# Performance work log

Measured on AMD Instinct MI355X. Metric: run time of the kernel, lower is better.

The kernel has to match this reference:

```python
import jax, jax.numpy as jnp
import numpy as np
import math

B, S, E, H = 2, 4096, 1024, 1024

def setup_inputs() -> dict:
    key = jax.random.key(0)
    ks = jax.random.split(key, 7)
    X = jax.random.normal(ks[0], (B, S, E), dtype=jnp.float32)
    attention_mask = jnp.ones((B, S, S), dtype=jnp.int32)
    sc = 1.0 / math.sqrt(E)
    Wq = jax.random.normal(ks[1], (H, E), dtype=jnp.float32) * sc
    Wk = jax.random.normal(ks[2], (H, E), dtype=jnp.float32) * sc
    Wv = jax.random.normal(ks[3], (H, E), dtype=jnp.float32) * sc
    bq = jnp.zeros((H,), dtype=jnp.float32)
    bk = jnp.zeros((H,), dtype=jnp.float32)
    bv = jnp.zeros((H,), dtype=jnp.float32)
    return {"X": X, "attention_mask": attention_mask,
            "Wq": Wq, "bq": bq, "Wk": Wk, "bk": bk, "Wv": Wv, "bv": bv}

def reference(X, attention_mask, Wq, bq, Wk, bk, Wv, bv):
    # Linear layers: y = x @ W^T + b (torch convention W is [out, in])
    Q = jnp.einsum('bse,he->bsh', X, Wq) + bq
    K = jnp.einsum('bse,he->bsh', X, Wk) + bk
    V = jnp.einsum('bse,he->bsh', X, Wv) + bv
    scale = 1.0 / math.sqrt(H)
    scores = jnp.einsum('bqh,bkh->bqk', Q, K) * scale  # [B,S,S]
    scores = jnp.where(attention_mask == 0, -jnp.inf, scores)
    # dropout (eval mode -> identity) would be applied here, BEFORE softmax
    weights = jax.nn.softmax(scores, axis=-1)
    out = jnp.einsum('bqk,bkh->bqh', weights, V)  # [B,S,H]
    return out
```

## Files before the change

kernel.cpp:

```cpp
#include <hip/hip_runtime.h>
#include <stdint.h>


typedef __bf16 bf16;
typedef __attribute__((ext_vector_type(4))) __bf16 bf16x4;
typedef __attribute__((ext_vector_type(8))) __bf16 bf16x8;
typedef __attribute__((ext_vector_type(4))) float f32x4;
typedef __attribute__((ext_vector_type(4))) int i32x4;

__device__ __forceinline__ void g2l16(const void* g, void* l) {
  __builtin_amdgcn_global_load_lds(
      (const __attribute__((address_space(1))) uint32_t*)g,
      (__attribute__((address_space(3))) uint32_t*)l, 16, 0, 0);
}

__global__ __launch_bounds__(256) void cvt_f32_bf16(
    const float* __restrict__ src, bf16* __restrict__ dst, int n) {
  const int i = (blockIdx.x * 256 + threadIdx.x) * 8;
  if (i >= n) return;
  f32x4 a = *(const f32x4*)(src + i);
  f32x4 b = *(const f32x4*)(src + i + 4);
  bf16x8 o;
#pragma unroll
  for (int e = 0; e < 4; ++e) { o[e] = (bf16)a[e]; o[4 + e] = (bf16)b[e]; }
  *(bf16x8*)(dst + i) = o;
}

__global__ __launch_bounds__(256) void cvt_w3(
    const float* __restrict__ Wq, const float* __restrict__ Wk,
    const float* __restrict__ Wv, bf16* __restrict__ dst) {
  const int i = (blockIdx.x * 256 + threadIdx.x) * 8;
  const int seg = i >> 20;
  const int off = i & 1048575;
  const float* src = (seg == 0) ? Wq : (seg == 1) ? Wk : Wv;
  f32x4 a = *(const f32x4*)(src + off);
  f32x4 b = *(const f32x4*)(src + off + 4);
  bf16x8 o;
#pragma unroll
  for (int e = 0; e < 4; ++e) { o[e] = (bf16)a[e]; o[4 + e] = (bf16)b[e]; }
  *(bf16x8*)(dst + i) = o;
}


__global__ __launch_bounds__(256, 2) void gemm_qkv(
    const bf16* __restrict__ Xb, const bf16* __restrict__ Wb3,
    const float* __restrict__ bq, const float* __restrict__ bk,
    const float* __restrict__ bv, bf16* __restrict__ QK,
    bf16* __restrict__ Vt)
{
  constexpr int K = 1024, N = 1024;
  __shared__ __align__(16) bf16 ldsA[128 * 64];
  __shared__ __align__(16) bf16 ldsB[128 * 64];

  const int tid  = threadIdx.x;
  const int lane = tid & 63;
  const int wave = tid >> 6;
  const int which = blockIdx.y >> 3;
  const int n0 = (blockIdx.y & 7) * 128;
  const int m0 = blockIdx.x * 128;
  const bf16* Bt = Wb3 + (size_t)which * 1048576;
  const float* bias = (which == 0) ? bq : ((which == 1) ? bk : bv);

  const int l15  = lane & 15;
  const int quad = lane >> 4;
  const int wm = (wave >> 1) * 64;
  const int wn = (wave & 1) * 64;
  const int sw = l15 & 7;

  f32x4 acc[4][4];
#pragma unroll
  for (int i = 0; i < 4; ++i)
#pragma unroll
    for (int j = 0; j < 4; ++j) acc[i][j] = f32x4{0.f, 0.f, 0.f, 0.f};

  const int srow = tid >> 3;
  const int scol = ((tid & 7) ^ (srow & 7)) * 8;
  const size_t a_base = (size_t)(m0 + srow) * K + scol;
  const size_t b_base = (size_t)(n0 + srow) * K + scol;
  const int lds_off = tid * 8;

  for (int kt = 0; kt < K; kt += 64) {
    const bf16* ga = Xb + a_base + kt;
    const bf16* gb = Bt + b_base + kt;
#pragma unroll
    for (int it = 0; it < 4; ++it) {
      g2l16(ga + (size_t)(it * 32) * K, &ldsA[lds_off + it * 2048]);
      g2l16(gb + (size_t)(it * 32) * K, &ldsB[lds_off + it * 2048]);
    }
    __syncthreads();
#pragma unroll
    for (int ks = 0; ks < 2; ++ks) {
      const int ch = ks * 4 + quad;
      bf16x8 af[4], bfg[4];
#pragma unroll
      for (int i = 0; i < 4; ++i)
        af[i] = *(const bf16x8*)&ldsA[(wm + i * 16 + l15) * 64 + (ch ^ sw) * 8];
#pragma unroll
      for (int j = 0; j < 4; ++j)
        bfg[j] = *(const bf16x8*)&ldsB[(wn + j * 16 + l15) * 64 + (ch ^ sw) * 8];
#pragma unroll
      for (int i = 0; i < 4; ++i)
#pragma unroll
        for (int j = 0; j < 4; ++j)
          acc[i][j] = __builtin_amdgcn_mfma_f32_16x16x32_bf16(
              af[i], bfg[j], acc[i][j], 0, 0, 0);
    }
    __syncthreads();
  }

  if (which < 2) {
    bf16* C = QK + (size_t)which * (size_t)(8192 * 1024);
#pragma unroll
    for (int i = 0; i < 4; ++i) {
#pragma unroll
      for (int j = 0; j < 4; ++j) {
        const int r = m0 + wm + i * 16 + quad * 4;
        const int c = n0 + wn + j * 16 + l15;
        const float bvv = bias[c];
        f32x4 v = acc[i][j];
#pragma unroll
        for (int reg = 0; reg < 4; ++reg)
          C[(size_t)(r + reg) * N + c] = (bf16)(v[reg] + bvv);
      }
    }
  } else {
#pragma unroll
    for (int i = 0; i < 4; ++i) {
#pragma unroll
      for (int j = 0; j < 4; ++j) {
        const int r = m0 + wm + i * 16 + quad * 4;
        const int c = n0 + wn + j * 16 + l15;
        const int b = r >> 12, s = r & 4095;
        const float bvv = bias[c];
        f32x4 v = acc[i][j];
        bf16x4 o;
#pragma unroll
        for (int reg = 0; reg < 4; ++reg) o[reg] = (bf16)(v[reg] + bvv);
        *(bf16x4*)&Vt[((size_t)(b * 1024 + c)) * 4096 + s] = o;
      }
    }
  }
}

template <typename CT>
__global__ __launch_bounds__(256, 2) void gemm_bt(
    const bf16* __restrict__ A, const bf16* __restrict__ Bt,
    CT* __restrict__ C, int M, int N, int K, long long bt_batch_stride,
    float scale)
{
  __shared__ __align__(16) bf16 ldsA[128 * 64];
  __shared__ __align__(16) bf16 ldsB[128 * 64];

  const int tid  = threadIdx.x;
  const int lane = tid & 63;
  const int wave = tid >> 6;
  const int m0 = blockIdx.x * 128;
  const int n0 = blockIdx.y * 128;
  const int batch = m0 >> 12;
  const bf16* Btb = Bt + (size_t)batch * (size_t)bt_batch_stride;

  const int l15  = lane & 15;
  const int quad = lane >> 4;
  const int wm = (wave >> 1) * 64;
  const int wn = (wave & 1) * 64;
  const int sw = l15 & 7;

  f32x4 acc[4][4];
#pragma unroll
  for (int i = 0; i < 4; ++i)
#pragma unroll
    for (int j = 0; j < 4; ++j) acc[i][j] = f32x4{0.f, 0.f, 0.f, 0.f};

  const int srow = tid >> 3;
  const int scol = ((tid & 7) ^ (srow & 7)) * 8;
  const size_t a_base = (size_t)(m0 + srow) * K + scol;
  const size_t b_base = (size_t)(n0 + srow) * K + scol;
  const int lds_off = tid * 8;

  for (int kt = 0; kt < K; kt += 64) {
    const bf16* ga = A + a_base + kt;
    const bf16* gb = Btb + b_base + kt;
#pragma unroll
    for (int it = 0; it < 4; ++it) {
      g2l16(ga + (size_t)(it * 32) * K, &ldsA[lds_off + it * 2048]);
      g2l16(gb + (size_t)(it * 32) * K, &ldsB[lds_off + it * 2048]);
    }
    __syncthreads();
#pragma unroll
    for (int ks = 0; ks < 2; ++ks) {
      const int ch = ks * 4 + quad;
      bf16x8 af[4], bfg[4];
#pragma unroll
      for (int i = 0; i < 4; ++i)
        af[i] = *(const bf16x8*)&ldsA[(wm + i * 16 + l15) * 64 + (ch ^ sw) * 8];
#pragma unroll
      for (int j = 0; j < 4; ++j)
        bfg[j] = *(const bf16x8*)&ldsB[(wn + j * 16 + l15) * 64 + (ch ^ sw) * 8];
#pragma unroll
      for (int i = 0; i < 4; ++i)
#pragma unroll
        for (int j = 0; j < 4; ++j)
          acc[i][j] = __builtin_amdgcn_mfma_f32_16x16x32_bf16(
              af[i], bfg[j], acc[i][j], 0, 0, 0);
    }
    __syncthreads();
  }

#pragma unroll
  for (int i = 0; i < 4; ++i) {
#pragma unroll
    for (int j = 0; j < 4; ++j) {
      const int r = m0 + wm + i * 16 + quad * 4;
      const int c = n0 + wn + j * 16 + l15;
      f32x4 v = acc[i][j];
#pragma unroll
      for (int reg = 0; reg < 4; ++reg)
        C[(size_t)(r + reg) * N + c] = (CT)(v[reg] * scale);
    }
  }
}

__global__ __launch_bounds__(256) void softmax_rows(
    bf16* __restrict__ Sc, const int* __restrict__ mask) {
  const int row = blockIdx.x;
  bf16* p = Sc + (size_t)row * 4096;
  const int* mrow = mask + (size_t)row * 4096;
  const int tid = threadIdx.x;
  const int wave = tid >> 6;

  const bf16x8* pv = (const bf16x8*)p;
  bf16x8 v0 = pv[tid * 2];
  bf16x8 v1 = pv[tid * 2 + 1];
  const i32x4* mv = (const i32x4*)mrow;
  i32x4 mk[4];
#pragma unroll
  for (int q = 0; q < 4; ++q) mk[q] = mv[tid * 4 + q];

  float x[16];
#pragma unroll
  for (int i = 0; i < 8; ++i) {
    x[i] = (float)v0[i];
    x[8 + i] = (float)v1[i];
  }
#pragma unroll
  for (int i = 0; i < 16; ++i)
    if (mk[i >> 2][i & 3] == 0) x[i] = -30000.0f;

  float m = -30000.0f;
#pragma unroll
  for (int i = 0; i < 16; ++i) m = fmaxf(m, x[i]);
#pragma unroll
  for (int off = 1; off < 64; off <<= 1) m = fmaxf(m, __shfl_xor(m, off));
  __shared__ float red[4];
  if ((tid & 63) == 0) red[wave] = m;
  __syncthreads();
  m = fmaxf(fmaxf(red[0], red[1]), fmaxf(red[2], red[3]));

  float s = 0.f;
#pragma unroll
  for (int i = 0; i < 16; ++i) {
    x[i] = __expf(x[i] - m);
    s += x[i];
  }
#pragma unroll
  for (int off = 1; off < 64; off <<= 1) s += __shfl_xor(s, off);
  __syncthreads();
  if ((tid & 63) == 0) red[wave] = s;
  __syncthreads();
  s = red[0] + red[1] + red[2] + red[3];
  const float inv = 1.0f / s;

  bf16x8 o0, o1;
#pragma unroll
  for (int i = 0; i < 8; ++i) {
    o0[i] = (bf16)(x[i] * inv);
    o1[i] = (bf16)(x[8 + i] * inv);
  }
  bf16x8* pw = (bf16x8*)p;
  pw[tid * 2] = o0;
  pw[tid * 2 + 1] = o1;
}

extern "C" void kernel_launch(void* const* d_in, const int* in_sizes, int n_in,
                              void* d_out, int out_size, void* d_ws,
                              size_t ws_size, hipStream_t stream) {
  const float* X   = (const float*)d_in[0];
  const int* mask  = (const int*)d_in[1];
  const float* Wq  = (const float*)d_in[2];
  const float* bq  = (const float*)d_in[3];
  const float* Wk  = (const float*)d_in[4];
  const float* bk  = (const float*)d_in[5];
  const float* Wv  = (const float*)d_in[6];
  const float* bv  = (const float*)d_in[7];
  float* out = (float*)d_out;

  const size_t QKV_ELEMS = (size_t)8192 * 1024;
  bf16* Q    = (bf16*)d_ws;
  bf16* Kb   = Q + QKV_ELEMS;
  bf16* X_bf = Kb + QKV_ELEMS;
  bf16* Vt   = X_bf + QKV_ELEMS;
  bf16* Sc   = Vt + QKV_ELEMS;
  bf16* W_bf = Sc;

  const dim3 blk(256);
  cvt_f32_bf16<<<dim3(4096), blk, 0, stream>>>(X, X_bf, 8388608);
  cvt_w3<<<dim3(1536), blk, 0, stream>>>(Wq, Wk, Wv, W_bf);
  gemm_qkv<<<dim3(64, 24), blk, 0, stream>>>(X_bf, W_bf, bq, bk, bv, Q, Vt);
  gemm_bt<bf16><<<dim3(64, 32), blk, 0, stream>>>(
      Q, Kb, Sc, 8192, 4096, 1024, 4096LL * 1024LL, 0.03125f);
  softmax_rows<<<dim3(8192), blk, 0, stream>>>(Sc, mask);
  gemm_bt<float><<<dim3(64, 8), blk, 0, stream>>>(
      Sc, Vt, out, 8192, 1024, 4096, 1024LL * 4096LL, 1.0f);
}
```

Measured before the change: 432.6 us.

## Fuse mask and exp into score GEMM epilogue, defer normalization to PV GEMM

```diff
diff --git a/kernel.cpp b/kernel.cpp
--- a/kernel.cpp
+++ b/kernel.cpp
@@ -6,7 +6,6 @@
 typedef __attribute__((ext_vector_type(4))) __bf16 bf16x4;
 typedef __attribute__((ext_vector_type(8))) __bf16 bf16x8;
 typedef __attribute__((ext_vector_type(4))) float f32x4;
-typedef __attribute__((ext_vector_type(4))) int i32x4;
 
 __device__ __forceinline__ void g2l16(const void* g, void* l) {
   __builtin_amdgcn_global_load_lds(
@@ -142,12 +141,12 @@
   }
 }
 
-template <typename CT>
-__global__ __launch_bounds__(256, 2) void gemm_bt(
+__global__ __launch_bounds__(256, 2) void gemm_scores(
     const bf16* __restrict__ A, const bf16* __restrict__ Bt,
-    CT* __restrict__ C, int M, int N, int K, long long bt_batch_stride,
-    float scale)
+    const int* __restrict__ mask, bf16* __restrict__ P,
+    float* __restrict__ row_sum)
 {
+  constexpr int N = 4096, K = 1024;
   __shared__ __align__(16) bf16 ldsA[128 * 64];
   __shared__ __align__(16) bf16 ldsB[128 * 64];
 
@@ -157,7 +156,7 @@
   const int m0 = blockIdx.x * 128;
   const int n0 = blockIdx.y * 128;
   const int batch = m0 >> 12;
-  const bf16* Btb = Bt + (size_t)batch * (size_t)bt_batch_stride;
+  const bf16* Btb = Bt + (size_t)batch * (size_t)(4096 * 1024);
 
   const int l15  = lane & 15;
   const int quad = lane >> 4;
@@ -208,77 +207,112 @@
 
 #pragma unroll
   for (int i = 0; i < 4; ++i) {
+    const int r = m0 + wm + i * 16 + quad * 4;
+    f32x4 rsum = f32x4{0.f, 0.f, 0.f, 0.f};
 #pragma unroll
     for (int j = 0; j < 4; ++j) {
-      const int r = m0 + wm + i * 16 + quad * 4;
       const int c = n0 + wn + j * 16 + l15;
       f32x4 v = acc[i][j];
 #pragma unroll
+      for (int reg = 0; reg < 4; ++reg) {
+        float e = __expf(v[reg] * 0.03125f);
+        if (mask[(size_t)(r + reg) * N + c] == 0) e = 0.f;
+        P[(size_t)(r + reg) * N + c] = (bf16)e;
+        rsum[reg] += e;
+      }
+    }
+#pragma unroll
+    for (int off = 1; off < 16; off <<= 1) {
+#pragma unroll
       for (int reg = 0; reg < 4; ++reg)
-        C[(size_t)(r + reg) * N + c] = (CT)(v[reg] * scale);
-    }
-  }
-}
-
-__global__ __launch_bounds__(256) void softmax_rows(
-    bf16* __restrict__ Sc, const int* __restrict__ mask) {
-  const int row = blockIdx.x;
-  bf16* p = Sc + (size_t)row * 4096;
-  const int* mrow = mask + (size_t)row * 4096;
-  const int tid = threadIdx.x;
+        rsum[reg] += __shfl_xor(rsum[reg], off);
+    }
+    if (l15 == 0) {
+#pragma unroll
+      for (int reg = 0; reg < 4; ++reg)
+        atomicAdd(&row_sum[r + reg], rsum[reg]);
+    }
+  }
+}
+
+__global__ __launch_bounds__(256, 2) void gemm_pv(
+    const bf16* __restrict__ A, const bf16* __restrict__ Bt,
+    const float* __restrict__ row_sum, float* __restrict__ C)
+{
+  constexpr int N = 1024, K = 4096;
+  __shared__ __align__(16) bf16 ldsA[128 * 64];
+  __shared__ __align__(16) bf16 ldsB[128 * 64];
+
+  const int tid  = threadIdx.x;
+  const int lane = tid & 63;
   const int wave = tid >> 6;
-
-  const bf16x8* pv = (const bf16x8*)p;
-  bf16x8 v0 = pv[tid * 2];
-  bf16x8 v1 = pv[tid * 2 + 1];
-  const i32x4* mv = (const i32x4*)mrow;
-  i32x4 mk[4];
-#pragma unroll
-  for (int q = 0; q < 4; ++q) mk[q] = mv[tid * 4 + q];
-
-  float x[16];
-#pragma unroll
-  for (int i = 0; i < 8; ++i) {
-    x[i] = (float)v0[i];
-    x[8 + i] = (float)v1[i];
-  }
-#pragma unroll
-  for (int i = 0; i < 16; ++i)
-    if (mk[i >> 2][i & 3] == 0) x[i] = -30000.0f;
-
-  float m = -30000.0f;
-#pragma unroll
-  for (int i = 0; i < 16; ++i) m = fmaxf(m, x[i]);
-#pragma unroll
-  for (int off = 1; off < 64; off <<= 1) m = fmaxf(m, __shfl_xor(m, off));
-  __shared__ float red[4];
-  if ((tid & 63) == 0) red[wave] = m;
-  __syncthreads();
-  m = fmaxf(fmaxf(red[0], red[1]), fmaxf(red[2], red[3]));
-
-  float s = 0.f;
-#pragma unroll
-  for (int i = 0; i < 16; ++i) {
-    x[i] = __expf(x[i] - m);
-    s += x[i];
-  }
-#pragma unroll
-  for (int off = 1; off < 64; off <<= 1) s += __shfl_xor(s, off);
-  __syncthreads();
-  if ((tid & 63) == 0) red[wave] = s;
-  __syncthreads();
-  s = red[0] + red[1] + red[2] + red[3];
-  const float inv = 1.0f / s;
-
-  bf16x8 o0, o1;
-#pragma unroll
-  for (int i = 0; i < 8; ++i) {
-    o0[i] = (bf16)(x[i] * inv);
-    o1[i] = (bf16)(x[8 + i] * inv);
-  }
-  bf16x8* pw = (bf16x8*)p;
-  pw[tid * 2] = o0;
-  pw[tid * 2 + 1] = o1;
+  const int m0 = blockIdx.x * 128;
+  const int n0 = blockIdx.y * 128;
+  const int batch = m0 >> 12;
+  const bf16* Btb = Bt + (size_t)batch * (size_t)(1024 * 4096);
+
+  const int l15  = lane & 15;
+  const int quad = lane >> 4;
+  const int wm = (wave >> 1) * 64;
+  const int wn = (wave & 1) * 64;
+  const int sw = l15 & 7;
+
+  f32x4 acc[4][4];
+#pragma unroll
+  for (int i = 0; i < 4; ++i)
+#pragma unroll
+    for (int j = 0; j < 4; ++j) acc[i][j] = f32x4{0.f, 0.f, 0.f, 0.f};
+
+  const int srow = tid >> 3;
+  const int scol = ((tid & 7) ^ (srow & 7)) * 8;
+  const size_t a_base = (size_t)(m0 + srow) * K + scol;
+  const size_t b_base = (size_t)(n0 + srow) * K + scol;
+  const int lds_off = tid * 8;
+
+  for (int kt = 0; kt < K; kt += 64) {
+    const bf16* ga = A + a_base + kt;
+    const bf16* gb = Btb + b_base + kt;
+#pragma unroll
+    for (int it = 0; it < 4; ++it) {
+      g2l16(ga + (size_t)(it * 32) * K, &ldsA[lds_off + it * 2048]);
+      g2l16(gb + (size_t)(it * 32) * K, &ldsB[lds_off + it * 2048]);
+    }
+    __syncthreads();
+#pragma unroll
+    for (int ks = 0; ks < 2; ++ks) {
+      const int ch = ks * 4 + quad;
+      bf16x8 af[4], bfg[4];
+#pragma unroll
+      for (int i = 0; i < 4; ++i)
+        af[i] = *(const bf16x8*)&ldsA[(wm + i * 16 + l15) * 64 + (ch ^ sw) * 8];
+#pragma unroll
+      for (int j = 0; j < 4; ++j)
+        bfg[j] = *(const bf16x8*)&ldsB[(wn + j * 16 + l15) * 64 + (ch ^ sw) * 8];
+#pragma unroll
+      for (int i = 0; i < 4; ++i)
+#pragma unroll
+        for (int j = 0; j < 4; ++j)
+          acc[i][j] = __builtin_amdgcn_mfma_f32_16x16x32_bf16(
+              af[i], bfg[j], acc[i][j], 0, 0, 0);
+    }
+    __syncthreads();
+  }
+
+#pragma unroll
+  for (int i = 0; i < 4; ++i) {
+    const int r = m0 + wm + i * 16 + quad * 4;
+    f32x4 inv;
+#pragma unroll
+    for (int reg = 0; reg < 4; ++reg) inv[reg] = 1.0f / row_sum[r + reg];
+#pragma unroll
+    for (int j = 0; j < 4; ++j) {
+      const int c = n0 + wn + j * 16 + l15;
+      f32x4 v = acc[i][j];
+#pragma unroll
+      for (int reg = 0; reg < 4; ++reg)
+        C[(size_t)(r + reg) * N + c] = v[reg] * inv[reg];
+    }
+  }
 }
 
 extern "C" void kernel_launch(void* const* d_in, const int* in_sizes, int n_in,
@@ -301,14 +335,13 @@
   bf16* Vt   = X_bf + QKV_ELEMS;
   bf16* Sc   = Vt + QKV_ELEMS;
   bf16* W_bf = Sc;
+  float* row_sum = (float*)X_bf;
 
   const dim3 blk(256);
   cvt_f32_bf16<<<dim3(4096), blk, 0, stream>>>(X, X_bf, 8388608);
   cvt_w3<<<dim3(1536), blk, 0, stream>>>(Wq, Wk, Wv, W_bf);
   gemm_qkv<<<dim3(64, 24), blk, 0, stream>>>(X_bf, W_bf, bq, bk, bv, Q, Vt);
-  gemm_bt<bf16><<<dim3(64, 32), blk, 0, stream>>>(
-      Q, Kb, Sc, 8192, 4096, 1024, 4096LL * 1024LL, 0.03125f);
-  softmax_rows<<<dim3(8192), blk, 0, stream>>>(Sc, mask);
-  gemm_bt<float><<<dim3(64, 8), blk, 0, stream>>>(
-      Sc, Vt, out, 8192, 1024, 4096, 1024LL * 4096LL, 1.0f);
-}
+  hipMemsetAsync(row_sum, 0, 8192 * sizeof(float), stream);
+  gemm_scores<<<dim3(64, 32), blk, 0, stream>>>(Q, Kb, mask, Sc, row_sum);
+  gemm_pv<<<dim3(64, 8), blk, 0, stream>>>(Sc, Vt, row_sum, out);
+}
```

Measured after the change: 427.4 us. Within noise of the previous version (-1.2%).
